# Optimization experiments

Hardware: AMD Instinct MI355X
Metric: run time of the kernel (lower is better)

The kernel has to match this reference:

```python
import jax, jax.numpy as jnp
import numpy as np

D_MODEL = 1024
N_HEADS = 16
B, T = 2, 2048


def setup_inputs() -> dict:
    key = jax.random.key(0)
    ks = jax.random.split(key, 5)
    scale = 1.0 / np.sqrt(D_MODEL)
    return {
        "x": jax.random.normal(ks[0], (B, T, D_MODEL), dtype=jnp.float32),
        "W_q": jax.random.normal(ks[1], (D_MODEL, D_MODEL), dtype=jnp.float32) * scale,
        "W_k": jax.random.normal(ks[2], (D_MODEL, D_MODEL), dtype=jnp.float32) * scale,
        "W_v": jax.random.normal(ks[3], (D_MODEL, D_MODEL), dtype=jnp.float32) * scale,
        "W_o": jax.random.normal(ks[4], (D_MODEL, D_MODEL), dtype=jnp.float32) * scale,
    }


def reference(x, W_q, W_k, W_v, W_o):
    Bn, Tn, D = x.shape
    H = N_HEADS
    Dh = D // H
    # nn.Linear(x) = x @ W.T ; weights stored as [out, in]
    q = (x @ W_q.T).reshape(Bn, Tn, H, Dh).transpose(0, 2, 1, 3)  # [B,H,T,Dh]
    k = (x @ W_k.T).reshape(Bn, Tn, H, Dh).transpose(0, 2, 1, 3)
    v = (x @ W_v.T).reshape(Bn, Tn, H, Dh).transpose(0, 2, 1, 3)
    scores = jnp.einsum("bhqd,bhkd->bhqk", q, k) / np.sqrt(Dh).astype(np.float32)
    attn = jax.nn.softmax(scores, axis=-1)  # [B,H,T,T]
    out = jnp.einsum("bhqk,bhkd->bhqd", attn, v)  # [B,H,T,Dh]
    out = out.transpose(0, 2, 1, 3).reshape(Bn, Tn, D)
    return out @ W_o.T
```

## Files before the change

kernel.cpp:

```cpp
#include <hip/hip_runtime.h>
#include <stdint.h>
#include <stddef.h>


typedef __bf16  bf16x8  __attribute__((ext_vector_type(8)));
typedef __bf16  bf16x4  __attribute__((ext_vector_type(4)));
typedef float   floatx4 __attribute__((ext_vector_type(4)));
typedef short   short4v __attribute__((ext_vector_type(4)));

#define DEV static __device__ __forceinline__

DEV void ld_g2l16(const void* g, void* l) {
    __builtin_amdgcn_global_load_lds(
        (__attribute__((address_space(1))) void*)g,
        (__attribute__((address_space(3))) void*)l,
        16, 0, 0);
}

DEV floatx4 mfma16(bf16x4 a, bf16x4 b, floatx4 c) {
#if defined(__HIP_DEVICE_COMPILE__)
    return __builtin_amdgcn_mfma_f32_16x16x16bf16_1k(
        __builtin_bit_cast(short4v, a), __builtin_bit_cast(short4v, b),
        c, 0, 0, 0);
#else
    (void)a; (void)b;
    return c;
#endif
}

#define WK_SCALE 0.18033688011112042f

__global__ __launch_bounds__(256) void cvt_all(
    const float* __restrict__ x,
    const float* __restrict__ wq, const float* __restrict__ wk,
    const float* __restrict__ wv, const float* __restrict__ wo,
    __bf16* __restrict__ xb,
    __bf16* __restrict__ wqb, __bf16* __restrict__ wkb,
    __bf16* __restrict__ wvb, __bf16* __restrict__ wob)
{
    unsigned u = blockIdx.x * 256u + threadIdx.x;
    const float* src;
    __bf16* dst;
    unsigned off;
    float mul = 1.0f;
    if (u < 1048576u) {
        src = x; dst = xb; off = u;
    } else {
        unsigned u2 = u - 1048576u;
        unsigned sel = u2 >> 18;
        off = u2 & 0x3FFFFu;
        src = (sel == 0) ? wq : (sel == 1) ? wk : (sel == 2) ? wv : wo;
        dst = (sel == 0) ? wqb : (sel == 1) ? wkb : (sel == 2) ? wvb : wob;
        if (sel == 1) mul = WK_SCALE;
    }
    float4 f = *(const float4*)(src + (size_t)off * 4);
    bf16x4 o = { (__bf16)(f.x * mul), (__bf16)(f.y * mul),
                 (__bf16)(f.z * mul), (__bf16)(f.w * mul) };
    *(bf16x4*)(dst + (size_t)off * 4) = o;
}

template<int BM, int NMAT, bool OUT_F32>
__global__ __launch_bounds__(256) void gemm_bt(
    const __bf16* __restrict__ A,
    const __bf16* __restrict__ B0, const __bf16* __restrict__ B1,
    const __bf16* __restrict__ B2,
    void* __restrict__ C0, void* __restrict__ C1, void* __restrict__ C2)
{
    constexpr int Kd = 1024;
    constexpr int N  = 1024;
    constexpr int MI = BM / 32;
    constexpr int NA = BM / 64;
    __shared__ __bf16 As[BM * 32];
    __shared__ __bf16 Bs[128 * 32];

    const int t    = threadIdx.x;
    const int wid  = __builtin_amdgcn_readfirstlane(t >> 6);
    const int lane = t & 63;
    const int quad = lane >> 4;
    const int l15  = lane & 15;

    const int bx  = blockIdx.x;
    const int mat = (NMAT > 1) ? (bx >> 3) : 0;
    const int bn  = (NMAT > 1) ? (bx & 7)  : bx;
    const int bm  = blockIdx.y;
    const __bf16* Bm = (mat == 0) ? B0 : (mat == 1) ? B1 : B2;

    const __bf16* pA[NA];
    const __bf16* pB[2];
#pragma unroll
    for (int i = 0; i < NA; ++i) {
        int c    = i * 256 + t;
        int row  = c >> 2;
        int g    = (c & 3) ^ ((row >> 1) & 3);
        pA[i] = A + (size_t)(bm * BM + row) * Kd + g * 8;
    }
#pragma unroll
    for (int i = 0; i < 2; ++i) {
        int c    = i * 256 + t;
        int row  = c >> 2;
        int g    = (c & 3) ^ ((row >> 1) & 3);
        pB[i] = Bm + (size_t)(bn * 128 + row) * Kd + g * 8;
    }

    const int wm = wid >> 1;
    const int wn = wid & 1;
    const int slotr = quad ^ ((l15 >> 1) & 3);

    floatx4 acc[MI][4];
    const floatx4 z = { 0.f, 0.f, 0.f, 0.f };
#pragma unroll
    for (int i = 0; i < MI; ++i)
#pragma unroll
        for (int j = 0; j < 4; ++j) acc[i][j] = z;

    for (int kb = 0; kb < Kd; kb += 32) {
        __syncthreads();
#pragma unroll
        for (int i = 0; i < NA; ++i)
            ld_g2l16(pA[i] + kb, (char*)As + i * 4096 + wid * 1024);
#pragma unroll
        for (int i = 0; i < 2; ++i)
            ld_g2l16(pB[i] + kb, (char*)Bs + i * 4096 + wid * 1024);
        __syncthreads();

        bf16x8 af[MI], bf[4];
#pragma unroll
        for (int i = 0; i < MI; ++i) {
            int rowA = wm * (BM / 2) + i * 16 + l15;
            af[i] = *(const bf16x8*)&As[rowA * 32 + slotr * 8];
        }
#pragma unroll
        for (int j = 0; j < 4; ++j) {
            int rowB = wn * 64 + j * 16 + l15;
            bf[j] = *(const bf16x8*)&Bs[rowB * 32 + slotr * 8];
        }
#pragma unroll
        for (int i = 0; i < MI; ++i)
#pragma unroll
            for (int j = 0; j < 4; ++j)
                acc[i][j] = __builtin_amdgcn_mfma_f32_16x16x32_bf16(
                    af[i], bf[j], acc[i][j], 0, 0, 0);
    }

    void* Cv = (mat == 0) ? C0 : (mat == 1) ? C1 : C2;
    const int row0 = bm * BM + wm * (BM / 2);
    const int col0 = bn * 128 + wn * 64;
#pragma unroll
    for (int i = 0; i < MI; ++i)
#pragma unroll
        for (int j = 0; j < 4; ++j)
#pragma unroll
            for (int r = 0; r < 4; ++r) {
                int grow = row0 + i * 16 + quad * 4 + r;
                int gcol = col0 + j * 16 + l15;
                if (OUT_F32)
                    ((float*)Cv)[(size_t)grow * N + gcol] = acc[i][j][r];
                else
                    ((__bf16*)Cv)[(size_t)grow * N + gcol] = (__bf16)acc[i][j][r];
            }
}

__global__ __launch_bounds__(256) void transpose_v(
    const __bf16* __restrict__ V, __bf16* __restrict__ Vt)
{
    __shared__ __bf16 tile[64 * 72];
    const int t  = threadIdx.x;
    const int kt = blockIdx.x;
    const int bh = blockIdx.y;
    const int b  = bh >> 4, h = bh & 15;

#pragma unroll
    for (int rr = 0; rr < 64; rr += 32) {
        int row = rr + (t >> 3), ch = t & 7;
        uint4 v = *(const uint4*)(V + (size_t)(b * 2048 + kt * 64 + row) * 1024
                                    + h * 64 + ch * 8);
        *(uint4*)&tile[row * 72 + ch * 8] = v;
    }
    __syncthreads();
#pragma unroll
    for (int dd = 0; dd < 64; dd += 32) {
        int d = dd + (t >> 3), ch = t & 7;
        bf16x8 val;
#pragma unroll
        for (int j = 0; j < 8; ++j) val[j] = tile[(ch * 8 + j) * 72 + d];
        *(bf16x8*)(Vt + (size_t)(bh * 64 + d) * 2048 + kt * 64 + ch * 8) = val;
    }
}

__global__ __launch_bounds__(256, 3) void flash_kernel(
    const __bf16* __restrict__ Q, const __bf16* __restrict__ K,
    const __bf16* __restrict__ Vt, __bf16* __restrict__ O)
{
    __shared__ __bf16 Qs[128 * 64];
    __shared__ __bf16 Ks[2][64 * 64];
    __shared__ __bf16 Vs[2][64 * 64];

    const int t    = threadIdx.x;
    const int wid  = __builtin_amdgcn_readfirstlane(t >> 6);
    const int lane = t & 63;
    const int quad = lane >> 4;
    const int l15  = lane & 15;
    const int qt   = blockIdx.x;
    const int bh   = blockIdx.y;
    const int b    = bh >> 4, h = bh & 15;

#pragma unroll
    for (int i = 0; i < 4; ++i) {
        int c = i * 256 + t;
        int row = c >> 3;
        int g   = (c & 7) ^ (row & 7);
        ld_g2l16(Q + (size_t)(b * 2048 + qt * 128 + row) * 1024 + h * 64 + g * 8,
                 (char*)Qs + i * 4096 + wid * 1024);
    }
#define ISSUE_KV(KT, BUF)                                                      \
    do {                                                                       \
        _Pragma("unroll")                                                      \
        for (int i_ = 0; i_ < 2; ++i_) {                                       \
            int c_ = i_ * 256 + t;                                             \
            int row_ = c_ >> 3;                                                \
            int g_   = (c_ & 7) ^ (row_ & 7);                                  \
            ld_g2l16(K + (size_t)(b * 2048 + (KT) * 64 + row_) * 1024          \
                         + h * 64 + g_ * 8,                                    \
                     (char*)Ks[BUF] + i_ * 4096 + wid * 1024);                 \
            ld_g2l16(Vt + (size_t)(bh * 64 + row_) * 2048 + (KT) * 64 + g_ * 8,\
                     (char*)Vs[BUF] + i_ * 4096 + wid * 1024);                 \
        }                                                                      \
    } while (0)

    ISSUE_KV(0, 0);
    __syncthreads();

    bf16x8 qf[2][2];
#pragma unroll
    for (int nb = 0; nb < 2; ++nb)
#pragma unroll
        for (int ks = 0; ks < 2; ++ks) {
            int row  = wid * 32 + nb * 16 + l15;
            int slot = (ks * 4 + quad) ^ (row & 7);
            qf[nb][ks] = *(const bf16x8*)&Qs[row * 64 + slot * 8];
        }

    const floatx4 z = { 0.f, 0.f, 0.f, 0.f };
    floatx4 o[2][4];
#pragma unroll
    for (int nb = 0; nb < 2; ++nb)
#pragma unroll
        for (int nd = 0; nd < 4; ++nd) o[nb][nd] = z;
    float lsum[2] = { 0.f, 0.f };

    for (int kt = 0; kt < 32; ++kt) {
        const int cur = kt & 1;
        if (kt) __syncthreads();
        if (kt < 31) ISSUE_KV(kt + 1, cur ^ 1);

#pragma unroll
        for (int kt16 = 0; kt16 < 4; ++kt16) {
            floatx4 s[2] = { z, z };
#pragma unroll
            for (int ks = 0; ks < 2; ++ks) {
                int rowk = kt16 * 16 + l15;
                int slot = (ks * 4 + quad) ^ (rowk & 7);
                bf16x8 kf = *(const bf16x8*)&Ks[cur][rowk * 64 + slot * 8];
#pragma unroll
                for (int nb = 0; nb < 2; ++nb)
                    s[nb] = __builtin_amdgcn_mfma_f32_16x16x32_bf16(
                        kf, qf[nb][ks], s[nb], 0, 0, 0);
            }
            bf16x4 pb[2];
#pragma unroll
            for (int nb = 0; nb < 2; ++nb) {
                float p0 = __builtin_amdgcn_exp2f(s[nb][0]);
                float p1 = __builtin_amdgcn_exp2f(s[nb][1]);
                float p2 = __builtin_amdgcn_exp2f(s[nb][2]);
                float p3 = __builtin_amdgcn_exp2f(s[nb][3]);
                lsum[nb] += (p0 + p1) + (p2 + p3);
                bf16x4 pw = { (__bf16)p0, (__bf16)p1, (__bf16)p2, (__bf16)p3 };
                pb[nb] = pw;
            }
#pragma unroll
            for (int nd = 0; nd < 4; ++nd) {
                int row  = nd * 16 + l15;
                int g    = kt16 * 2 + (quad >> 1);
                int slot = g ^ (row & 7);
                bf16x4 va = *(const bf16x4*)
                    &Vs[cur][row * 64 + slot * 8 + (quad & 1) * 4];
#pragma unroll
                for (int nb = 0; nb < 2; ++nb)
                    o[nb][nd] = mfma16(va, pb[nb], o[nb][nd]);
            }
        }
    }
#undef ISSUE_KV

#pragma unroll
    for (int nb = 0; nb < 2; ++nb) {
        lsum[nb] += __shfl_xor(lsum[nb], 16);
        lsum[nb] += __shfl_xor(lsum[nb], 32);
    }
#pragma unroll
    for (int nb = 0; nb < 2; ++nb) {
        float inv = 1.f / lsum[nb];
        int token = qt * 128 + wid * 32 + nb * 16 + l15;
#pragma unroll
        for (int nd = 0; nd < 4; ++nd) {
            bf16x4 ov = { (__bf16)(o[nb][nd][0] * inv),
                          (__bf16)(o[nb][nd][1] * inv),
                          (__bf16)(o[nb][nd][2] * inv),
                          (__bf16)(o[nb][nd][3] * inv) };
            *(bf16x4*)(O + (size_t)(b * 2048 + token) * 1024
                         + h * 64 + nd * 16 + quad * 4) = ov;
        }
    }
}

extern "C" void kernel_launch(void* const* d_in, const int* in_sizes, int n_in,
                              void* d_out, int out_size, void* d_ws, size_t ws_size,
                              hipStream_t stream)
{
    const float* x  = (const float*)d_in[0];
    const float* wq = (const float*)d_in[1];
    const float* wk = (const float*)d_in[2];
    const float* wv = (const float*)d_in[3];
    const float* wo = (const float*)d_in[4];

    char* ws = (char*)d_ws;
    __bf16* xb  = (__bf16*)(ws + 0);
    __bf16* wqb = (__bf16*)(ws + 8388608);
    __bf16* wkb = (__bf16*)(ws + 10485760);
    __bf16* wvb = (__bf16*)(ws + 12582912);
    __bf16* wob = (__bf16*)(ws + 14680064);
    __bf16* Qb  = (__bf16*)(ws + 16777216);
    __bf16* Kb  = (__bf16*)(ws + 25165824);
    __bf16* Vb  = (__bf16*)(ws + 33554432);
    __bf16* Vtb = (__bf16*)(ws + 41943040);
    __bf16* Ob  = xb;

    cvt_all<<<8192, 256, 0, stream>>>(x, wq, wk, wv, wo, xb, wqb, wkb, wvb, wob);

    gemm_bt<128, 3, false><<<dim3(24, 32), 256, 0, stream>>>(
        xb, wqb, wkb, wvb, (void*)Qb, (void*)Kb, (void*)Vb);

    transpose_v<<<dim3(32, 32), 256, 0, stream>>>(Vb, Vtb);

    flash_kernel<<<dim3(16, 32), 256, 0, stream>>>(Qb, Kb, Vtb, Ob);

    gemm_bt<64, 1, true><<<dim3(8, 64), 256, 0, stream>>>(
        Ob, wob, nullptr, nullptr, d_out, nullptr, nullptr);
}
```

Before: 188.9 us.

## Double-buffer GEMM LDS loads and compute softmax row sums via MFMA

The projection GEMM now double-buffers its A/B shared-memory tiles, prefetching the next k-slice while computing on the current one, and drops one barrier per iteration. In the flash kernel, row sums of the bf16 probabilities are accumulated with an MFMA against a ones vector instead of scalar adds and a cross-lane shuffle reduction. LDS offsets are precomputed and loops are unrolled by two. Launch-bound occupancy hints change for both kernels. This adds LDS use in the GEMM and extra MFMA work in attention. The denominator is now summed from bf16-rounded probabilities, a slight numeric change.

```diff
diff --git a/kernel.cpp b/kernel.cpp
--- a/kernel.cpp
+++ b/kernel.cpp
@@ -60,7 +60,7 @@
 }
 
 template<int BM, int NMAT, bool OUT_F32>
-__global__ __launch_bounds__(256) void gemm_bt(
+__global__ __launch_bounds__(256, 3) void gemm_bt(
     const __bf16* __restrict__ A,
     const __bf16* __restrict__ B0, const __bf16* __restrict__ B1,
     const __bf16* __restrict__ B2,
@@ -70,8 +70,8 @@
     constexpr int N  = 1024;
     constexpr int MI = BM / 32;
     constexpr int NA = BM / 64;
-    __shared__ __bf16 As[BM * 32];
-    __shared__ __bf16 Bs[128 * 32];
+    __shared__ __bf16 As[2][BM * 32];
+    __shared__ __bf16 Bs[2][128 * 32];
 
     const int t    = threadIdx.x;
     const int wid  = __builtin_amdgcn_readfirstlane(t >> 6);
@@ -113,26 +113,37 @@
 #pragma unroll
         for (int j = 0; j < 4; ++j) acc[i][j] = z;
 
-    for (int kb = 0; kb < Kd; kb += 32) {
+#pragma unroll
+    for (int i = 0; i < NA; ++i)
+        ld_g2l16(pA[i], (char*)As[0] + i * 4096 + wid * 1024);
+#pragma unroll
+    for (int i = 0; i < 2; ++i)
+        ld_g2l16(pB[i], (char*)Bs[0] + i * 4096 + wid * 1024);
+
+#pragma unroll 2
+    for (int it = 0; it < 32; ++it) {
+        const int cur = it & 1;
         __syncthreads();
-#pragma unroll
-        for (int i = 0; i < NA; ++i)
-            ld_g2l16(pA[i] + kb, (char*)As + i * 4096 + wid * 1024);
-#pragma unroll
-        for (int i = 0; i < 2; ++i)
-            ld_g2l16(pB[i] + kb, (char*)Bs + i * 4096 + wid * 1024);
-        __syncthreads();
+        if (it < 31) {
+            int kb = (it + 1) * 32;
+#pragma unroll
+            for (int i = 0; i < NA; ++i)
+                ld_g2l16(pA[i] + kb, (char*)As[cur ^ 1] + i * 4096 + wid * 1024);
+#pragma unroll
+            for (int i = 0; i < 2; ++i)
+                ld_g2l16(pB[i] + kb, (char*)Bs[cur ^ 1] + i * 4096 + wid * 1024);
+        }
 
         bf16x8 af[MI], bf[4];
 #pragma unroll
         for (int i = 0; i < MI; ++i) {
             int rowA = wm * (BM / 2) + i * 16 + l15;
-            af[i] = *(const bf16x8*)&As[rowA * 32 + slotr * 8];
+            af[i] = *(const bf16x8*)&As[cur][rowA * 32 + slotr * 8];
         }
 #pragma unroll
         for (int j = 0; j < 4; ++j) {
             int rowB = wn * 64 + j * 16 + l15;
-            bf[j] = *(const bf16x8*)&Bs[rowB * 32 + slotr * 8];
+            bf[j] = *(const bf16x8*)&Bs[cur][rowB * 32 + slotr * 8];
         }
 #pragma unroll
         for (int i = 0; i < MI; ++i)
@@ -187,7 +198,7 @@
     }
 }
 
-__global__ __launch_bounds__(256, 3) void flash_kernel(
+__global__ __launch_bounds__(256, 2) void flash_kernel(
     const __bf16* __restrict__ Q, const __bf16* __restrict__ K,
     const __bf16* __restrict__ Vt, __bf16* __restrict__ O)
 {
@@ -240,27 +251,39 @@
             qf[nb][ks] = *(const bf16x8*)&Qs[row * 64 + slot * 8];
         }
 
+    int koff[2];
+#pragma unroll
+    for (int ks = 0; ks < 2; ++ks)
+        koff[ks] = l15 * 128 + (((ks * 4 + quad) ^ (l15 & 7)) << 4);
+    int voff[4];
+#pragma unroll
+    for (int k16 = 0; k16 < 4; ++k16)
+        voff[k16] = l15 * 128 + (((k16 * 2 + (quad >> 1)) ^ (l15 & 7)) << 4)
+                  + (quad & 1) * 8;
+
     const floatx4 z = { 0.f, 0.f, 0.f, 0.f };
     floatx4 o[2][4];
 #pragma unroll
     for (int nb = 0; nb < 2; ++nb)
 #pragma unroll
         for (int nd = 0; nd < 4; ++nd) o[nb][nd] = z;
-    float lsum[2] = { 0.f, 0.f };
-
+    floatx4 ls[2] = { z, z };
+    const bf16x4 ones = { (__bf16)1.f, (__bf16)1.f, (__bf16)1.f, (__bf16)1.f };
+
+#pragma unroll 2
     for (int kt = 0; kt < 32; ++kt) {
         const int cur = kt & 1;
         if (kt) __syncthreads();
         if (kt < 31) ISSUE_KV(kt + 1, cur ^ 1);
 
+        const char* kbase = (const char*)Ks[cur];
+        const char* vbase = (const char*)Vs[cur];
 #pragma unroll
         for (int kt16 = 0; kt16 < 4; ++kt16) {
             floatx4 s[2] = { z, z };
 #pragma unroll
             for (int ks = 0; ks < 2; ++ks) {
-                int rowk = kt16 * 16 + l15;
-                int slot = (ks * 4 + quad) ^ (rowk & 7);
-                bf16x8 kf = *(const bf16x8*)&Ks[cur][rowk * 64 + slot * 8];
+                bf16x8 kf = *(const bf16x8*)(kbase + kt16 * 2048 + koff[ks]);
 #pragma unroll
                 for (int nb = 0; nb < 2; ++nb)
                     s[nb] = __builtin_amdgcn_mfma_f32_16x16x32_bf16(
@@ -269,21 +292,16 @@
             bf16x4 pb[2];
 #pragma unroll
             for (int nb = 0; nb < 2; ++nb) {
-                float p0 = __builtin_amdgcn_exp2f(s[nb][0]);
-                float p1 = __builtin_amdgcn_exp2f(s[nb][1]);
-                float p2 = __builtin_amdgcn_exp2f(s[nb][2]);
-                float p3 = __builtin_amdgcn_exp2f(s[nb][3]);
-                lsum[nb] += (p0 + p1) + (p2 + p3);
-                bf16x4 pw = { (__bf16)p0, (__bf16)p1, (__bf16)p2, (__bf16)p3 };
+                bf16x4 pw = { (__bf16)__builtin_amdgcn_exp2f(s[nb][0]),
+                              (__bf16)__builtin_amdgcn_exp2f(s[nb][1]),
+                              (__bf16)__builtin_amdgcn_exp2f(s[nb][2]),
+                              (__bf16)__builtin_amdgcn_exp2f(s[nb][3]) };
                 pb[nb] = pw;
+                ls[nb] = mfma16(ones, pw, ls[nb]);
             }
 #pragma unroll
             for (int nd = 0; nd < 4; ++nd) {
-                int row  = nd * 16 + l15;
-                int g    = kt16 * 2 + (quad >> 1);
-                int slot = g ^ (row & 7);
-                bf16x4 va = *(const bf16x4*)
-                    &Vs[cur][row * 64 + slot * 8 + (quad & 1) * 4];
+                bf16x4 va = *(const bf16x4*)(vbase + nd * 2048 + voff[kt16]);
 #pragma unroll
                 for (int nb = 0; nb < 2; ++nb)
                     o[nb][nd] = mfma16(va, pb[nb], o[nb][nd]);
@@ -294,12 +312,7 @@
 
 #pragma unroll
     for (int nb = 0; nb < 2; ++nb) {
-        lsum[nb] += __shfl_xor(lsum[nb], 16);
-        lsum[nb] += __shfl_xor(lsum[nb], 32);
-    }
-#pragma unroll
-    for (int nb = 0; nb < 2; ++nb) {
-        float inv = 1.f / lsum[nb];
+        float inv = 1.f / ls[nb][0];
         int token = qt * 128 + wid * 32 + nb * 16 + l15;
 #pragma unroll
         for (int nd = 0; nd < 4; ++nd) {
```

Result: slower. 203.0 us (+7.5%).

## Use 8 waves per flash block with 16 query rows per wave

Applied to the files above, without the earlier changes.

The flash attention block moves from 4 waves each owning 32 query rows to 8 waves each owning 16 rows, with 512 threads per block. Each thread now issues one K and one V async load per tile instead of two. The LDS offsets for K and V are precomputed once, and the kt loop is unrolled by two. The goal is more waves to hide latency and less register pressure per wave, at the cost of each K/V fragment read from LDS being reused by only one MFMA row-block instead of two, which doubles LDS read traffic per FLOP.

```diff
diff --git a/kernel.cpp b/kernel.cpp
--- a/kernel.cpp
+++ b/kernel.cpp
@@ -187,7 +187,7 @@
     }
 }
 
-__global__ __launch_bounds__(256, 3) void flash_kernel(
+__global__ __launch_bounds__(512, 4) void flash_kernel(
     const __bf16* __restrict__ Q, const __bf16* __restrict__ K,
     const __bf16* __restrict__ Vt, __bf16* __restrict__ O)
 {
@@ -205,111 +205,92 @@
     const int b    = bh >> 4, h = bh & 15;
 
 #pragma unroll
-    for (int i = 0; i < 4; ++i) {
-        int c = i * 256 + t;
+    for (int i = 0; i < 2; ++i) {
+        int c = i * 512 + t;
         int row = c >> 3;
         int g   = (c & 7) ^ (row & 7);
         ld_g2l16(Q + (size_t)(b * 2048 + qt * 128 + row) * 1024 + h * 64 + g * 8,
-                 (char*)Qs + i * 4096 + wid * 1024);
+                 (char*)Qs + i * 8192 + wid * 1024);
     }
 #define ISSUE_KV(KT, BUF)                                                      \
     do {                                                                       \
-        _Pragma("unroll")                                                      \
-        for (int i_ = 0; i_ < 2; ++i_) {                                       \
-            int c_ = i_ * 256 + t;                                             \
-            int row_ = c_ >> 3;                                                \
-            int g_   = (c_ & 7) ^ (row_ & 7);                                  \
-            ld_g2l16(K + (size_t)(b * 2048 + (KT) * 64 + row_) * 1024          \
-                         + h * 64 + g_ * 8,                                    \
-                     (char*)Ks[BUF] + i_ * 4096 + wid * 1024);                 \
-            ld_g2l16(Vt + (size_t)(bh * 64 + row_) * 2048 + (KT) * 64 + g_ * 8,\
-                     (char*)Vs[BUF] + i_ * 4096 + wid * 1024);                 \
-        }                                                                      \
+        int row_ = t >> 3;                                                     \
+        int g_   = (t & 7) ^ (row_ & 7);                                       \
+        ld_g2l16(K + (size_t)(b * 2048 + (KT) * 64 + row_) * 1024              \
+                     + h * 64 + g_ * 8,                                        \
+                 (char*)Ks[BUF] + wid * 1024);                                 \
+        ld_g2l16(Vt + (size_t)(bh * 64 + row_) * 2048 + (KT) * 64 + g_ * 8,    \
+                 (char*)Vs[BUF] + wid * 1024);                                 \
     } while (0)
 
     ISSUE_KV(0, 0);
     __syncthreads();
 
-    bf16x8 qf[2][2];
-#pragma unroll
-    for (int nb = 0; nb < 2; ++nb)
-#pragma unroll
-        for (int ks = 0; ks < 2; ++ks) {
-            int row  = wid * 32 + nb * 16 + l15;
-            int slot = (ks * 4 + quad) ^ (row & 7);
-            qf[nb][ks] = *(const bf16x8*)&Qs[row * 64 + slot * 8];
-        }
+    bf16x8 qf[2];
+#pragma unroll
+    for (int ks = 0; ks < 2; ++ks) {
+        int row  = wid * 16 + l15;
+        int slot = (ks * 4 + quad) ^ (l15 & 7);
+        qf[ks] = *(const bf16x8*)&Qs[row * 64 + slot * 8];
+    }
+
+    int koff[2];
+#pragma unroll
+    for (int ks = 0; ks < 2; ++ks)
+        koff[ks] = l15 * 128 + (((ks * 4 + quad) ^ (l15 & 7)) << 4);
+    int voff[4];
+#pragma unroll
+    for (int k16 = 0; k16 < 4; ++k16)
+        voff[k16] = l15 * 128 + (((k16 * 2 + (quad >> 1)) ^ (l15 & 7)) << 4)
+                  + (quad & 1) * 8;
 
     const floatx4 z = { 0.f, 0.f, 0.f, 0.f };
-    floatx4 o[2][4];
-#pragma unroll
-    for (int nb = 0; nb < 2; ++nb)
-#pragma unroll
-        for (int nd = 0; nd < 4; ++nd) o[nb][nd] = z;
-    float lsum[2] = { 0.f, 0.f };
-
+    floatx4 o[4] = { z, z, z, z };
+    float lsum = 0.f;
+
+#pragma unroll 2
     for (int kt = 0; kt < 32; ++kt) {
         const int cur = kt & 1;
         if (kt) __syncthreads();
         if (kt < 31) ISSUE_KV(kt + 1, cur ^ 1);
 
+        const char* kbase = (const char*)Ks[cur];
+        const char* vbase = (const char*)Vs[cur];
 #pragma unroll
         for (int kt16 = 0; kt16 < 4; ++kt16) {
-            floatx4 s[2] = { z, z };
+            floatx4 s = z;
 #pragma unroll
             for (int ks = 0; ks < 2; ++ks) {
-                int rowk = kt16 * 16 + l15;
-                int slot = (ks * 4 + quad) ^ (rowk & 7);
-                bf16x8 kf = *(const bf16x8*)&Ks[cur][rowk * 64 + slot * 8];
-#pragma unroll
-                for (int nb = 0; nb < 2; ++nb)
-                    s[nb] = __builtin_amdgcn_mfma_f32_16x16x32_bf16(
-                        kf, qf[nb][ks], s[nb], 0, 0, 0);
+                bf16x8 kf = *(const bf16x8*)(kbase + kt16 * 2048 + koff[ks]);
+                s = __builtin_amdgcn_mfma_f32_16x16x32_bf16(kf, qf[ks], s, 0, 0, 0);
             }
-            bf16x4 pb[2];
-#pragma unroll
-            for (int nb = 0; nb < 2; ++nb) {
-                float p0 = __builtin_amdgcn_exp2f(s[nb][0]);
-                float p1 = __builtin_amdgcn_exp2f(s[nb][1]);
-                float p2 = __builtin_amdgcn_exp2f(s[nb][2]);
-                float p3 = __builtin_amdgcn_exp2f(s[nb][3]);
-                lsum[nb] += (p0 + p1) + (p2 + p3);
-                bf16x4 pw = { (__bf16)p0, (__bf16)p1, (__bf16)p2, (__bf16)p3 };
-                pb[nb] = pw;
-            }
+            float p0 = __builtin_amdgcn_exp2f(s[0]);
+            float p1 = __builtin_amdgcn_exp2f(s[1]);
+            float p2 = __builtin_amdgcn_exp2f(s[2]);
+            float p3 = __builtin_amdgcn_exp2f(s[3]);
+            lsum += (p0 + p1) + (p2 + p3);
+            bf16x4 pb = { (__bf16)p0, (__bf16)p1, (__bf16)p2, (__bf16)p3 };
 #pragma unroll
             for (int nd = 0; nd < 4; ++nd) {
-                int row  = nd * 16 + l15;
-                int g    = kt16 * 2 + (quad >> 1);
-                int slot = g ^ (row & 7);
-                bf16x4 va = *(const bf16x4*)
-                    &Vs[cur][row * 64 + slot * 8 + (quad & 1) * 4];
-#pragma unroll
-                for (int nb = 0; nb < 2; ++nb)
-                    o[nb][nd] = mfma16(va, pb[nb], o[nb][nd]);
+                bf16x4 va = *(const bf16x4*)(vbase + nd * 2048 + voff[kt16]);
+                o[nd] = mfma16(va, pb, o[nd]);
             }
         }
     }
 #undef ISSUE_KV
 
-#pragma unroll
-    for (int nb = 0; nb < 2; ++nb) {
-        lsum[nb] += __shfl_xor(lsum[nb], 16);
-        lsum[nb] += __shfl_xor(lsum[nb], 32);
-    }
-#pragma unroll
-    for (int nb = 0; nb < 2; ++nb) {
-        float inv = 1.f / lsum[nb];
-        int token = qt * 128 + wid * 32 + nb * 16 + l15;
-#pragma unroll
-        for (int nd = 0; nd < 4; ++nd) {
-            bf16x4 ov = { (__bf16)(o[nb][nd][0] * inv),
-                          (__bf16)(o[nb][nd][1] * inv),
-                          (__bf16)(o[nb][nd][2] * inv),
-                          (__bf16)(o[nb][nd][3] * inv) };
-            *(bf16x4*)(O + (size_t)(b * 2048 + token) * 1024
-                         + h * 64 + nd * 16 + quad * 4) = ov;
-        }
+    lsum += __shfl_xor(lsum, 16);
+    lsum += __shfl_xor(lsum, 32);
+    float inv = 1.f / lsum;
+    int token = qt * 128 + wid * 16 + l15;
+#pragma unroll
+    for (int nd = 0; nd < 4; ++nd) {
+        bf16x4 ov = { (__bf16)(o[nd][0] * inv),
+                      (__bf16)(o[nd][1] * inv),
+                      (__bf16)(o[nd][2] * inv),
+                      (__bf16)(o[nd][3] * inv) };
+        *(bf16x4*)(O + (size_t)(b * 2048 + token) * 1024
+                     + h * 64 + nd * 16 + quad * 4) = ov;
     }
 }
 
@@ -342,7 +323,7 @@
 
     transpose_v<<<dim3(32, 32), 256, 0, stream>>>(Vb, Vtb);
 
-    flash_kernel<<<dim3(16, 32), 256, 0, stream>>>(Qb, Kb, Vtb, Ob);
+    flash_kernel<<<dim3(16, 32), 512, 0, stream>>>(Qb, Kb, Vtb, Ob);
 
     gemm_bt<64, 1, true><<<dim3(8, 64), 256, 0, stream>>>(
         Ob, wob, nullptr, nullptr, d_out, nullptr, nullptr);
```

New measurement: 193.7 us. 2.5% more time.

## Split flash attention KV range across two wave groups per block

Applied to the files above, without the earlier changes.

The flash kernel now launches 512 threads per block. Two halves of four waves each process disjoint halves of the key/value sequence for the same 128 query rows, and their partial outputs and row sums are combined through shared memory at the end. This doubles waves per block and halves the serial KV loop length, aiming to improve latency hiding and occupancy on the 512-block grid. It also precomputes swizzled LDS offsets to cut address arithmetic. The cost is more shared memory for the extra KV buffers, a final reduction with two extra barriers, and a launch bound asking for four blocks per CU, which may pressure registers.

```diff
diff --git a/kernel.cpp b/kernel.cpp
--- a/kernel.cpp
+++ b/kernel.cpp
@@ -187,16 +187,18 @@
     }
 }
 
-__global__ __launch_bounds__(256, 3) void flash_kernel(
+__global__ __launch_bounds__(512, 4) void flash_kernel(
     const __bf16* __restrict__ Q, const __bf16* __restrict__ K,
     const __bf16* __restrict__ Vt, __bf16* __restrict__ O)
 {
     __shared__ __bf16 Qs[128 * 64];
-    __shared__ __bf16 Ks[2][64 * 64];
-    __shared__ __bf16 Vs[2][64 * 64];
+    __shared__ __bf16 Ks[2][2][64 * 64];
+    __shared__ __bf16 Vs[2][2][64 * 64];
 
     const int t    = threadIdx.x;
     const int wid  = __builtin_amdgcn_readfirstlane(t >> 6);
+    const int half = wid >> 2;
+    const int wsub = wid & 3;
     const int lane = t & 63;
     const int quad = lane >> 4;
     const int l15  = lane & 15;
@@ -205,26 +207,28 @@
     const int b    = bh >> 4, h = bh & 15;
 
 #pragma unroll
-    for (int i = 0; i < 4; ++i) {
-        int c = i * 256 + t;
+    for (int i = 0; i < 2; ++i) {
+        int c = i * 512 + t;
         int row = c >> 3;
         int g   = (c & 7) ^ (row & 7);
         ld_g2l16(Q + (size_t)(b * 2048 + qt * 128 + row) * 1024 + h * 64 + g * 8,
-                 (char*)Qs + i * 4096 + wid * 1024);
-    }
-#define ISSUE_KV(KT, BUF)                                                      \
+                 (char*)Qs + i * 8192 + wid * 1024);
+    }
+#define ISSUE_KV(IT, BUF)                                                      \
     do {                                                                       \
-        _Pragma("unroll")                                                      \
-        for (int i_ = 0; i_ < 2; ++i_) {                                       \
-            int c_ = i_ * 256 + t;                                             \
-            int row_ = c_ >> 3;                                                \
-            int g_   = (c_ & 7) ^ (row_ & 7);                                  \
-            ld_g2l16(K + (size_t)(b * 2048 + (KT) * 64 + row_) * 1024          \
-                         + h * 64 + g_ * 8,                                    \
-                     (char*)Ks[BUF] + i_ * 4096 + wid * 1024);                 \
-            ld_g2l16(Vt + (size_t)(bh * 64 + row_) * 2048 + (KT) * 64 + g_ * 8,\
-                     (char*)Vs[BUF] + i_ * 4096 + wid * 1024);                 \
-        }                                                                      \
+        int row_ = t >> 3;                                                     \
+        int g_   = (t & 7) ^ (row_ & 7);                                       \
+        ld_g2l16(K + (size_t)(b * 2048 + (IT) * 64 + row_) * 1024              \
+                     + h * 64 + g_ * 8,                                        \
+                 (char*)Ks[0][BUF] + wid * 1024);                              \
+        ld_g2l16(K + (size_t)(b * 2048 + (16 + (IT)) * 64 + row_) * 1024       \
+                     + h * 64 + g_ * 8,                                        \
+                 (char*)Ks[1][BUF] + wid * 1024);                              \
+        ld_g2l16(Vt + (size_t)(bh * 64 + row_) * 2048 + (IT) * 64 + g_ * 8,    \
+                 (char*)Vs[0][BUF] + wid * 1024);                              \
+        ld_g2l16(Vt + (size_t)(bh * 64 + row_) * 2048 + (16 + (IT)) * 64       \
+                     + g_ * 8,                                                 \
+                 (char*)Vs[1][BUF] + wid * 1024);                              \
     } while (0)
 
     ISSUE_KV(0, 0);
@@ -235,11 +239,21 @@
     for (int nb = 0; nb < 2; ++nb)
 #pragma unroll
         for (int ks = 0; ks < 2; ++ks) {
-            int row  = wid * 32 + nb * 16 + l15;
+            int row  = wsub * 32 + nb * 16 + l15;
             int slot = (ks * 4 + quad) ^ (row & 7);
             qf[nb][ks] = *(const bf16x8*)&Qs[row * 64 + slot * 8];
         }
 
+    int koff[2];
+#pragma unroll
+    for (int ks = 0; ks < 2; ++ks)
+        koff[ks] = l15 * 128 + (((ks * 4 + quad) ^ (l15 & 7)) << 4);
+    int voff[4];
+#pragma unroll
+    for (int k16 = 0; k16 < 4; ++k16)
+        voff[k16] = l15 * 128 + (((k16 * 2 + (quad >> 1)) ^ (l15 & 7)) << 4)
+                  + (quad & 1) * 8;
+
     const floatx4 z = { 0.f, 0.f, 0.f, 0.f };
     floatx4 o[2][4];
 #pragma unroll
@@ -248,19 +262,20 @@
         for (int nd = 0; nd < 4; ++nd) o[nb][nd] = z;
     float lsum[2] = { 0.f, 0.f };
 
-    for (int kt = 0; kt < 32; ++kt) {
-        const int cur = kt & 1;
-        if (kt) __syncthreads();
-        if (kt < 31) ISSUE_KV(kt + 1, cur ^ 1);
-
+#pragma unroll 2
+    for (int it = 0; it < 16; ++it) {
+        const int cur = it & 1;
+        if (it) __syncthreads();
+        if (it < 15) ISSUE_KV(it + 1, cur ^ 1);
+
+        const char* kbase = (const char*)Ks[half][cur];
+        const char* vbase = (const char*)Vs[half][cur];
 #pragma unroll
         for (int kt16 = 0; kt16 < 4; ++kt16) {
             floatx4 s[2] = { z, z };
 #pragma unroll
             for (int ks = 0; ks < 2; ++ks) {
-                int rowk = kt16 * 16 + l15;
-                int slot = (ks * 4 + quad) ^ (rowk & 7);
-                bf16x8 kf = *(const bf16x8*)&Ks[cur][rowk * 64 + slot * 8];
+                bf16x8 kf = *(const bf16x8*)(kbase + kt16 * 2048 + koff[ks]);
 #pragma unroll
                 for (int nb = 0; nb < 2; ++nb)
                     s[nb] = __builtin_amdgcn_mfma_f32_16x16x32_bf16(
@@ -279,11 +294,7 @@
             }
 #pragma unroll
             for (int nd = 0; nd < 4; ++nd) {
-                int row  = nd * 16 + l15;
-                int g    = kt16 * 2 + (quad >> 1);
-                int slot = g ^ (row & 7);
-                bf16x4 va = *(const bf16x4*)
-                    &Vs[cur][row * 64 + slot * 8 + (quad & 1) * 4];
+                bf16x4 va = *(const bf16x4*)(vbase + nd * 2048 + voff[kt16]);
 #pragma unroll
                 for (int nb = 0; nb < 2; ++nb)
                     o[nb][nd] = mfma16(va, pb[nb], o[nb][nd]);
@@ -292,23 +303,48 @@
     }
 #undef ISSUE_KV
 
-#pragma unroll
-    for (int nb = 0; nb < 2; ++nb) {
-        lsum[nb] += __shfl_xor(lsum[nb], 16);
-        lsum[nb] += __shfl_xor(lsum[nb], 32);
-    }
-#pragma unroll
-    for (int nb = 0; nb < 2; ++nb) {
-        float inv = 1.f / lsum[nb];
-        int token = qt * 128 + wid * 32 + nb * 16 + l15;
-#pragma unroll
-        for (int nd = 0; nd < 4; ++nd) {
-            bf16x4 ov = { (__bf16)(o[nb][nd][0] * inv),
-                          (__bf16)(o[nb][nd][1] * inv),
-                          (__bf16)(o[nb][nd][2] * inv),
-                          (__bf16)(o[nb][nd][3] * inv) };
-            *(bf16x4*)(O + (size_t)(b * 2048 + token) * 1024
-                         + h * 64 + nd * 16 + quad * 4) = ov;
+    __syncthreads();
+    float* comb  = (float*)&Ks[0][0][0];
+    float* lcomb = (float*)&Vs[0][0][0];
+    if (half == 1) {
+        float* my = comb + wsub * 2048;
+#pragma unroll
+        for (int nb = 0; nb < 2; ++nb)
+#pragma unroll
+            for (int nd = 0; nd < 4; ++nd)
+                *(floatx4*)(my + (nb * 4 + nd) * 256 + lane * 4) = o[nb][nd];
+        lcomb[wsub * 128 + lane]      = lsum[0];
+        lcomb[wsub * 128 + 64 + lane] = lsum[1];
+    }
+    __syncthreads();
+    if (half == 0) {
+        float* pr = comb + wsub * 2048;
+#pragma unroll
+        for (int nb = 0; nb < 2; ++nb)
+#pragma unroll
+            for (int nd = 0; nd < 4; ++nd)
+                o[nb][nd] += *(const floatx4*)(pr + (nb * 4 + nd) * 256 + lane * 4);
+        lsum[0] += lcomb[wsub * 128 + lane];
+        lsum[1] += lcomb[wsub * 128 + 64 + lane];
+
+#pragma unroll
+        for (int nb = 0; nb < 2; ++nb) {
+            lsum[nb] += __shfl_xor(lsum[nb], 16);
+            lsum[nb] += __shfl_xor(lsum[nb], 32);
+        }
+#pragma unroll
+        for (int nb = 0; nb < 2; ++nb) {
+            float inv = 1.f / lsum[nb];
+            int token = qt * 128 + wsub * 32 + nb * 16 + l15;
+#pragma unroll
+            for (int nd = 0; nd < 4; ++nd) {
+                bf16x4 ov = { (__bf16)(o[nb][nd][0] * inv),
+                              (__bf16)(o[nb][nd][1] * inv),
+                              (__bf16)(o[nb][nd][2] * inv),
+                              (__bf16)(o[nb][nd][3] * inv) };
+                *(bf16x4*)(O + (size_t)(b * 2048 + token) * 1024
+                             + h * 64 + nd * 16 + quad * 4) = ov;
+            }
         }
     }
 }
@@ -342,7 +378,7 @@
 
     transpose_v<<<dim3(32, 32), 256, 0, stream>>>(Vb, Vtb);
 
-    flash_kernel<<<dim3(16, 32), 256, 0, stream>>>(Qb, Kb, Vtb, Ob);
+    flash_kernel<<<dim3(16, 32), 512, 0, stream>>>(Qb, Kb, Vtb, Ob);
 
     gemm_bt<64, 1, true><<<dim3(8, 64), 256, 0, stream>>>(
         Ob, wob, nullptr, nullptr, d_out, nullptr, nullptr);
```

New measurement: 186.1 us. About the same (-1.5%).
